# Kernel optimization log

Hardware: AMD Instinct MI355X
Metric: run time of the kernel (lower is better)

## Reference

```python
import jax, jax.numpy as jnp
import numpy as np

HIDDEN = 1024
FFN = 4096
NUM_EXPERTS = 8
TOKENS = 4096


def setup_inputs() -> dict:
    key = jax.random.key(0)
    k1, k2, k3, k4 = jax.random.split(key, 4)
    x = jax.random.normal(k1, (TOKENS, HIDDEN), dtype=jnp.float32)
    router_weight = jax.random.normal(k2, (HIDDEN, NUM_EXPERTS), dtype=jnp.float32) * 0.02
    w1 = jax.random.normal(k3, (HIDDEN, FFN * NUM_EXPERTS), dtype=jnp.float32) * 0.02
    w2 = jax.random.normal(k4, (FFN * NUM_EXPERTS, HIDDEN), dtype=jnp.float32) * 0.02
    return {"x": x, "router_weight": router_weight, "w1": w1, "w2": w2, "top_k": 2}


def reference(x, router_weight, w1, w2, top_k):
    T, H = x.shape
    E = router_weight.shape[1]
    F = w1.shape[1] // E

    # Router: fp32 logits -> softmax -> top-k gating (sparse gates in dense [T, E] form)
    logits = x.astype(jnp.float32) @ router_weight  # [T, E]
    probs = jax.nn.softmax(logits, axis=-1)
    top_vals, top_idx = jax.lax.top_k(probs, top_k)  # [T, k]
    gates = jnp.zeros((T, E), dtype=probs.dtype).at[
        jnp.arange(T)[:, None], top_idx
    ].set(top_vals)  # [T, E], zero for non-selected experts

    # Per-expert FFN (expert-blocked weight layout: columns [e*F:(e+1)*F])
    w1e = w1.reshape(H, E, F)          # [H, E, F]
    w2e = w2.reshape(E, F, H)          # [E, F, H]
    h = jax.nn.gelu(jnp.einsum('th,hef->etf', x, w1e), approximate=False)  # [E, T, F]
    y = jnp.einsum('etf,efh->eth', h, w2e)  # [E, T, H]

    # Combine: gate-weighted sum over experts
    out = jnp.einsum('te,eth->th', gates.astype(y.dtype), y)  # [T, H]
    return out
```

## Files before the change

kernel.cpp:

```cpp
#include <hip/hip_runtime.h>
#include <hip/hip_bf16.h>

#define T_TOKENS 4096
#define HID 1024
#define FFN_ 4096
#define NE 8
#define MAXROWS 9216
#define MAXTILES 72
#define KSPLIT2 2

typedef unsigned short u16;
typedef __bf16 bf16x8 __attribute__((ext_vector_type(8)));
typedef float f32x4 __attribute__((ext_vector_type(4)));
typedef u16 u16x8 __attribute__((ext_vector_type(8)));

__device__ __forceinline__ u16 f2bf(float f) {
  __hip_bfloat16 h = __float2bfloat16(f);
  return *reinterpret_cast<u16*>(&h);
}

__device__ __forceinline__ void gload16(const void* g, void* l) {
  __builtin_amdgcn_global_load_lds(
      (const __attribute__((address_space(1))) void*)g,
      (__attribute__((address_space(3))) void*)l, 16, 0, 0);
}

#define WAIT_VM8() asm volatile("s_waitcnt vmcnt(8)" ::: "memory")
#define WAIT_VM0() asm volatile("s_waitcnt vmcnt(0)" ::: "memory")
#define BARRIER()  asm volatile("s_barrier" ::: "memory")

__global__ __launch_bounds__(256) void router_kernel(
    const float* __restrict__ x, const float* __restrict__ rw,
    int* __restrict__ sel, float* __restrict__ gsel) {
  int token = blockIdx.x * 4 + (threadIdx.x >> 6);
  int lane = threadIdx.x & 63;
  const float* xr = x + (size_t)token * HID;
  float acc[8];
#pragma unroll
  for (int e = 0; e < 8; e++) acc[e] = 0.f;
  for (int h = lane; h < HID; h += 64) {
    float xv = xr[h];
    float4 r0 = *(const float4*)(rw + h * 8);
    float4 r1 = *(const float4*)(rw + h * 8 + 4);
    acc[0] += xv * r0.x; acc[1] += xv * r0.y; acc[2] += xv * r0.z; acc[3] += xv * r0.w;
    acc[4] += xv * r1.x; acc[5] += xv * r1.y; acc[6] += xv * r1.z; acc[7] += xv * r1.w;
  }
#pragma unroll
  for (int e = 0; e < 8; e++) {
#pragma unroll
    for (int o = 32; o > 0; o >>= 1) acc[e] += __shfl_down(acc[e], o);
  }
  if (lane == 0) {
    float mx = acc[0];
#pragma unroll
    for (int e = 1; e < 8; e++) mx = fmaxf(mx, acc[e]);
    float p[8], s = 0.f;
#pragma unroll
    for (int e = 0; e < 8; e++) { p[e] = expf(acc[e] - mx); s += p[e]; }
    float v0 = -1.f; int i0 = 0;
#pragma unroll
    for (int e = 0; e < 8; e++) if (p[e] > v0) { v0 = p[e]; i0 = e; }
    float v1 = -1.f; int i1 = 0;
#pragma unroll
    for (int e = 0; e < 8; e++) if (e != i0 && p[e] > v1) { v1 = p[e]; i1 = e; }
    float inv = 1.f / s;
    sel[token * 2] = i0;     gsel[token * 2] = v0 * inv;
    sel[token * 2 + 1] = i1; gsel[token * 2 + 1] = v1 * inv;
  }
}

__global__ __launch_bounds__(256) void hist_kernel(const int* __restrict__ sel,
                                                   int* __restrict__ counts) {
  __shared__ int lc[NE];
  if (threadIdx.x < NE) lc[threadIdx.x] = 0;
  __syncthreads();
  int p = blockIdx.x * 256 + threadIdx.x;
  atomicAdd(&lc[sel[p]], 1);
  __syncthreads();
  if (threadIdx.x < NE) atomicAdd(&counts[threadIdx.x], lc[threadIdx.x]);
}

__global__ void base_kernel(const int* __restrict__ counts, int* __restrict__ cursor,
                            int* __restrict__ tilemap) {
  if (threadIdx.x == 0) {
    int base = 0;
    for (int e = 0; e < NE; e++) {
      cursor[e] = base;
      int padded = (base + counts[e] + 127) & ~127;
      for (int t = base >> 7; t < (padded >> 7); t++) tilemap[t] = e;
      base = padded;
    }
    for (int t = base >> 7; t < MAXTILES; t++) tilemap[t] = 0;
  }
}

__global__ __launch_bounds__(256) void fill_kernel(int* __restrict__ perm,
                                                   float* __restrict__ grow) {
  int i = blockIdx.x * 256 + threadIdx.x;
  if (i < MAXROWS) { perm[i] = -1; grow[i] = 0.f; }
}

__global__ __launch_bounds__(256) void scatter_kernel(
    const int* __restrict__ sel, const float* __restrict__ gsel,
    int* __restrict__ cursor, int* __restrict__ perm, float* __restrict__ grow) {
  int p = blockIdx.x * 256 + threadIdx.x;
  int e = sel[p];
  int pos = atomicAdd(&cursor[e], 1);
  perm[pos] = p >> 1;
  grow[pos] = gsel[p];
}

__global__ __launch_bounds__(256) void convert_x(const float* __restrict__ x, u16* __restrict__ xb) {
  int i = (blockIdx.x * 256 + threadIdx.x) * 8;
  float4 a = *(const float4*)(x + i);
  float4 b = *(const float4*)(x + i + 4);
  u16x8 o;
  o[0] = f2bf(a.x); o[1] = f2bf(a.y); o[2] = f2bf(a.z); o[3] = f2bf(a.w);
  o[4] = f2bf(b.x); o[5] = f2bf(b.y); o[6] = f2bf(b.z); o[7] = f2bf(b.w);
  *(u16x8*)(xb + i) = o;
}

__global__ __launch_bounds__(256) void transpose_w1(const float* __restrict__ w1, u16* __restrict__ w1t) {
  __shared__ float tile[64][65];
  int c0 = blockIdx.x * 64;
  int r0 = blockIdx.y * 64;
  int t = threadIdx.x;
  int ci = (t & 15) * 4;
  int ri = t >> 4;
#pragma unroll
  for (int rr = 0; rr < 64; rr += 16) {
    float4 v = *(const float4*)(w1 + (size_t)(r0 + ri + rr) * 32768 + c0 + ci);
    tile[ri + rr][ci] = v.x; tile[ri + rr][ci + 1] = v.y;
    tile[ri + rr][ci + 2] = v.z; tile[ri + rr][ci + 3] = v.w;
  }
  __syncthreads();
  int j = t >> 2;
  int q = t & 3;
  u16x8 o0, o1;
#pragma unroll
  for (int k = 0; k < 8; k++) o0[k] = f2bf(tile[q * 16 + k][j]);
#pragma unroll
  for (int k = 0; k < 8; k++) o1[k] = f2bf(tile[q * 16 + 8 + k][j]);
  u16* dst = w1t + (size_t)(c0 + j) * 1024 + r0 + q * 16;
  *(u16x8*)dst = o0;
  *(u16x8*)(dst + 8) = o1;
}

__global__ __launch_bounds__(256) void transpose_w2(const float* __restrict__ w2, u16* __restrict__ w2t) {
  __shared__ float tile[64][65];
  int fb = blockIdx.x;
  int h0 = blockIdx.y * 64;
  int e = fb >> 6;
  int f0 = (fb & 63) * 64;
  int t = threadIdx.x;
  int ci = (t & 15) * 4;
  int ri = t >> 4;
#pragma unroll
  for (int rr = 0; rr < 64; rr += 16) {
    float4 v = *(const float4*)(w2 + (size_t)(fb * 64 + ri + rr) * 1024 + h0 + ci);
    tile[ri + rr][ci] = v.x; tile[ri + rr][ci + 1] = v.y;
    tile[ri + rr][ci + 2] = v.z; tile[ri + rr][ci + 3] = v.w;
  }
  __syncthreads();
  int j = t >> 2;
  int q = t & 3;
  u16x8 o0, o1;
#pragma unroll
  for (int k = 0; k < 8; k++) o0[k] = f2bf(tile[q * 16 + k][j]);
#pragma unroll
  for (int k = 0; k < 8; k++) o1[k] = f2bf(tile[q * 16 + 8 + k][j]);
  u16* dst = w2t + (size_t)e * 4194304 + (size_t)(h0 + j) * 4096 + f0 + q * 16;
  *(u16x8*)dst = o0;
  *(u16x8*)(dst + 8) = o1;
}

__global__ __launch_bounds__(256) void gemm1_kernel(
    const u16* __restrict__ xb, const u16* __restrict__ w1t,
    const int* __restrict__ perm, const float* __restrict__ grow,
    const int* __restrict__ tilemap, u16* __restrict__ hbuf,
    const u16* __restrict__ zp) {
  int mt = blockIdx.x, nt = blockIdx.y;
  int e = tilemap[mt];
  int row0 = mt * 128;
  int t = threadIdx.x, lane = t & 63, wave = t >> 6;
  __shared__ u16 As[2][128 * 64], Bs[2][128 * 64];

  const u16* asrc[4]; int astep[4];
  const u16* bsrc[4];
#pragma unroll
  for (int i = 0; i < 4; i++) {
    int chunk = i * 256 + t, row = chunk >> 3, c = chunk & 7;
    int cs = c ^ (row & 7);
    int tok = perm[row0 + row];
    if (tok >= 0) { asrc[i] = xb + (size_t)tok * 1024 + cs * 8; astep[i] = 64; }
    else { asrc[i] = zp + cs * 8; astep[i] = 0; }
    bsrc[i] = w1t + (size_t)e * 4194304 + (size_t)(nt * 128 + row) * 1024 + cs * 8;
  }

  f32x4 acc[4][4] = {};
  int wm = (wave >> 1) * 64, wn = (wave & 1) * 64;
  int r = lane & 15, kg = lane >> 4;

  auto stage = [&](int p) {
#pragma unroll
    for (int i = 0; i < 4; i++)
      gload16(asrc[i], (char*)&As[p][0] + i * 4096 + wave * 1024);
#pragma unroll
    for (int i = 0; i < 4; i++)
      gload16(bsrc[i], (char*)&Bs[p][0] + i * 4096 + wave * 1024);
#pragma unroll
    for (int i = 0; i < 4; i++) { asrc[i] += astep[i]; bsrc[i] += 64; }
  };
  auto compute = [&](int p) {
#pragma unroll
    for (int kk = 0; kk < 2; kk++) {
      bf16x8 af[4], bfr[4];
      int kb = kk * 64 + kg * 16;
#pragma unroll
      for (int mi = 0; mi < 4; mi++) {
        int rr = wm + mi * 16 + r;
        af[mi] = *(const bf16x8*)((const char*)&As[p][0] + rr * 128 + (kb ^ ((rr & 7) << 4)));
      }
#pragma unroll
      for (int ni = 0; ni < 4; ni++) {
        int rr = wn + ni * 16 + r;
        bfr[ni] = *(const bf16x8*)((const char*)&Bs[p][0] + rr * 128 + (kb ^ ((rr & 7) << 4)));
      }
#pragma unroll
      for (int mi = 0; mi < 4; mi++)
#pragma unroll
        for (int ni = 0; ni < 4; ni++)
          acc[mi][ni] = __builtin_amdgcn_mfma_f32_16x16x32_bf16(af[mi], bfr[ni], acc[mi][ni], 0, 0, 0);
    }
  };

  stage(0);
  stage(1);
  for (int ks = 0; ks < 15; ks++) {
    WAIT_VM8();
    BARRIER();
    compute(ks & 1);
    BARRIER();
    if (ks < 14) stage(ks & 1);
  }
  WAIT_VM0();
  BARRIER();
  compute(1);

  float g[4][4];
#pragma unroll
  for (int mi = 0; mi < 4; mi++)
#pragma unroll
    for (int j = 0; j < 4; j++)
      g[mi][j] = grow[row0 + wm + mi * 16 + kg * 4 + j];
#pragma unroll
  for (int mi = 0; mi < 4; mi++)
#pragma unroll
    for (int ni = 0; ni < 4; ni++)
#pragma unroll
      for (int j = 0; j < 4; j++) {
        int rl = wm + mi * 16 + kg * 4 + j;
        int col = nt * 128 + wn + ni * 16 + r;
        float v = acc[mi][ni][j];
        float ge = 0.5f * v * (1.0f + erff(v * 0.7071067811865475f)) * g[mi][j];
        hbuf[(size_t)(row0 + rl) * 4096 + col] = f2bf(ge);
      }
}

__global__ __launch_bounds__(256) void gemm2_kernel(
    const u16* __restrict__ hbuf, const u16* __restrict__ w2t,
    const int* __restrict__ perm, const int* __restrict__ tilemap,
    float* __restrict__ out) {
  int mt = blockIdx.x, nt = blockIdx.y;
  int ksplit = blockIdx.z;
  int e = tilemap[mt];
  int row0 = mt * 128;
  int t = threadIdx.x, lane = t & 63, wave = t >> 6;
  __shared__ u16 As[2][128 * 64], Bs[2][128 * 64];

  const u16* asrc[4];
  const u16* bsrc[4];
#pragma unroll
  for (int i = 0; i < 4; i++) {
    int chunk = i * 256 + t, row = chunk >> 3, c = chunk & 7;
    int cs = c ^ (row & 7);
    asrc[i] = hbuf + (size_t)(row0 + row) * 4096 + (size_t)ksplit * 2048 + cs * 8;
    bsrc[i] = w2t + (size_t)e * 4194304 + (size_t)(nt * 128 + row) * 4096 + (size_t)ksplit * 2048 + cs * 8;
  }

  f32x4 acc[4][4] = {};
  int wm = (wave >> 1) * 64, wn = (wave & 1) * 64;
  int r = lane & 15, kg = lane >> 4;

  auto stage = [&](int p) {
#pragma unroll
    for (int i = 0; i < 4; i++)
      gload16(asrc[i], (char*)&As[p][0] + i * 4096 + wave * 1024);
#pragma unroll
    for (int i = 0; i < 4; i++)
      gload16(bsrc[i], (char*)&Bs[p][0] + i * 4096 + wave * 1024);
#pragma unroll
    for (int i = 0; i < 4; i++) { asrc[i] += 64; bsrc[i] += 64; }
  };
  auto compute = [&](int p) {
#pragma unroll
    for (int kk = 0; kk < 2; kk++) {
      bf16x8 af[4], bfr[4];
      int kb = kk * 64 + kg * 16;
#pragma unroll
      for (int mi = 0; mi < 4; mi++) {
        int rr = wm + mi * 16 + r;
        af[mi] = *(const bf16x8*)((const char*)&As[p][0] + rr * 128 + (kb ^ ((rr & 7) << 4)));
      }
#pragma unroll
      for (int ni = 0; ni < 4; ni++) {
        int rr = wn + ni * 16 + r;
        bfr[ni] = *(const bf16x8*)((const char*)&Bs[p][0] + rr * 128 + (kb ^ ((rr & 7) << 4)));
      }
#pragma unroll
      for (int mi = 0; mi < 4; mi++)
#pragma unroll
        for (int ni = 0; ni < 4; ni++)
          acc[mi][ni] = __builtin_amdgcn_mfma_f32_16x16x32_bf16(af[mi], bfr[ni], acc[mi][ni], 0, 0, 0);
    }
  };

  stage(0);
  stage(1);
  for (int ks = 0; ks < 31; ks++) {
    WAIT_VM8();
    BARRIER();
    compute(ks & 1);
    BARRIER();
    if (ks < 30) stage(ks & 1);
  }
  WAIT_VM0();
  BARRIER();
  compute(1);

  int tok[4][4];
#pragma unroll
  for (int mi = 0; mi < 4; mi++)
#pragma unroll
    for (int j = 0; j < 4; j++)
      tok[mi][j] = perm[row0 + wm + mi * 16 + kg * 4 + j];
#pragma unroll
  for (int mi = 0; mi < 4; mi++)
#pragma unroll
    for (int ni = 0; ni < 4; ni++)
#pragma unroll
      for (int j = 0; j < 4; j++) {
        if (tok[mi][j] >= 0) {
          int col = nt * 128 + wn + ni * 16 + r;
          atomicAdd(out + (size_t)tok[mi][j] * 1024 + col, acc[mi][ni][j]);
        }
      }
}

extern "C" void kernel_launch(void* const* d_in, const int* in_sizes, int n_in,
                              void* d_out, int out_size, void* d_ws, size_t ws_size,
                              hipStream_t stream) {
  const float* x  = (const float*)d_in[0];
  const float* rw = (const float*)d_in[1];
  const float* w1 = (const float*)d_in[2];
  const float* w2 = (const float*)d_in[3];
  float* out = (float*)d_out;
  char* ws = (char*)d_ws;

  size_t off = 0;
  auto take = [&](size_t n) { char* p = ws + off; off += (n + 255) & ~255ull; return p; };
  u16* w1t   = (u16*)take(8ull * 4096 * 1024 * 2);
  u16* w2t   = (u16*)take(8ull * 4096 * 1024 * 2);
  u16* xb    = (u16*)take((size_t)T_TOKENS * HID * 2);
  u16* hbuf  = (u16*)take((size_t)MAXROWS * FFN_ * 2);
  int* sel   = (int*)take(T_TOKENS * 2 * 4);
  float* gsel = (float*)take(T_TOKENS * 2 * 4);
  int* perm  = (int*)take(MAXROWS * 4);
  float* grow = (float*)take(MAXROWS * 4);
  int* tmap  = (int*)take(MAXTILES * 4);
  int* counts = (int*)take(NE * 4);
  int* cursor = (int*)take(NE * 4);
  u16* zp    = (u16*)take(4096);

  hipMemsetAsync(zp, 0, 4096, stream);
  hipMemsetAsync(counts, 0, NE * 4, stream);
  hipMemsetAsync(out, 0, (size_t)T_TOKENS * HID * 4, stream);

  convert_x<<<dim3(T_TOKENS * HID / (256 * 8)), 256, 0, stream>>>(x, xb);
  transpose_w1<<<dim3(512, 16), 256, 0, stream>>>(w1, w1t);
  transpose_w2<<<dim3(512, 16), 256, 0, stream>>>(w2, w2t);
  router_kernel<<<dim3(T_TOKENS / 4), 256, 0, stream>>>(x, rw, sel, gsel);
  hist_kernel<<<dim3(T_TOKENS * 2 / 256), 256, 0, stream>>>(sel, counts);
  base_kernel<<<dim3(1), 64, 0, stream>>>(counts, cursor, tmap);
  fill_kernel<<<dim3((MAXROWS + 255) / 256), 256, 0, stream>>>(perm, grow);
  scatter_kernel<<<dim3(T_TOKENS * 2 / 256), 256, 0, stream>>>(sel, gsel, cursor, perm, grow);
  gemm1_kernel<<<dim3(MAXTILES, 32), 256, 0, stream>>>(xb, w1t, perm, grow, tmap, hbuf, zp);
  gemm2_kernel<<<dim3(MAXTILES, 8, KSPLIT2), 256, 0, stream>>>(hbuf, w2t, perm, tmap, out);
}
```

Measured before the change: 438.0 us.

## Enlarge grouped GEMM tiles to 256x256 with 8 waves and XCD-aware block mapping

Both expert GEMMs move from 128x128 tiles with 4 waves to 256x256 tiles with 8 waves, so each loaded A/B byte feeds more MFMAs and global/LDS traffic per flop drops. Expert padding goes to 256 rows, and a 1D grid is remapped so blocks sharing an M-tile land on the same XCD for L2 reuse. GEMM2 now splits K four ways instead of two. It also adds s_setprio around MFMA bursts and moves the barrier inside compute. Costs are more padding waste, double the LDS per block, heavier register pressure (a 32-accumulator array), and more atomic adds into the output.

```diff
diff --git a/kernel.cpp b/kernel.cpp
--- a/kernel.cpp
+++ b/kernel.cpp
@@ -5,9 +5,8 @@
 #define HID 1024
 #define FFN_ 4096
 #define NE 8
-#define MAXROWS 9216
-#define MAXTILES 72
-#define KSPLIT2 2
+#define MAXROWS 10240
+#define MAXTILES 40
 
 typedef unsigned short u16;
 typedef __bf16 bf16x8 __attribute__((ext_vector_type(8)));
@@ -86,11 +85,11 @@
     int base = 0;
     for (int e = 0; e < NE; e++) {
       cursor[e] = base;
-      int padded = (base + counts[e] + 127) & ~127;
-      for (int t = base >> 7; t < (padded >> 7); t++) tilemap[t] = e;
+      int padded = (base + counts[e] + 255) & ~255;
+      for (int t = base >> 8; t < (padded >> 8); t++) tilemap[t] = e;
       base = padded;
     }
-    for (int t = base >> 7; t < MAXTILES; t++) tilemap[t] = 0;
+    for (int t = base >> 8; t < MAXTILES; t++) tilemap[t] = 0;
   }
 }
 
@@ -174,184 +173,225 @@
   *(u16x8*)(dst + 8) = o1;
 }
 
-__global__ __launch_bounds__(256) void gemm1_kernel(
+__global__ __launch_bounds__(512, 2) void gemm1_kernel(
     const u16* __restrict__ xb, const u16* __restrict__ w1t,
     const int* __restrict__ perm, const float* __restrict__ grow,
     const int* __restrict__ tilemap, u16* __restrict__ hbuf,
     const u16* __restrict__ zp) {
-  int mt = blockIdx.x, nt = blockIdx.y;
+  int bid = blockIdx.x;
+  int xcd = bid & 7, pos = bid >> 3;
+  int nt = pos / 5;
+  int mt = xcd * 5 + (pos - nt * 5);
   int e = tilemap[mt];
-  int row0 = mt * 128;
+  int row0 = mt * 256;
   int t = threadIdx.x, lane = t & 63, wave = t >> 6;
-  __shared__ u16 As[2][128 * 64], Bs[2][128 * 64];
+  __shared__ u16 As[2][256 * 64], Bs[2][256 * 64];
 
   const u16* asrc[4]; int astep[4];
   const u16* bsrc[4];
 #pragma unroll
   for (int i = 0; i < 4; i++) {
-    int chunk = i * 256 + t, row = chunk >> 3, c = chunk & 7;
+    int chunk = i * 512 + t, row = chunk >> 3, c = chunk & 7;
     int cs = c ^ (row & 7);
     int tok = perm[row0 + row];
     if (tok >= 0) { asrc[i] = xb + (size_t)tok * 1024 + cs * 8; astep[i] = 64; }
     else { asrc[i] = zp + cs * 8; astep[i] = 0; }
-    bsrc[i] = w1t + (size_t)e * 4194304 + (size_t)(nt * 128 + row) * 1024 + cs * 8;
-  }
-
-  f32x4 acc[4][4] = {};
-  int wm = (wave >> 1) * 64, wn = (wave & 1) * 64;
+    bsrc[i] = w1t + (size_t)e * 4194304 + (size_t)(nt * 256 + row) * 1024 + cs * 8;
+  }
+
+  f32x4 acc[8][4] = {};
+  int wm = wave >> 2, wn = wave & 3;
   int r = lane & 15, kg = lane >> 4;
 
   auto stage = [&](int p) {
 #pragma unroll
     for (int i = 0; i < 4; i++)
-      gload16(asrc[i], (char*)&As[p][0] + i * 4096 + wave * 1024);
+      gload16(asrc[i], (char*)&As[p][0] + i * 8192 + wave * 1024);
 #pragma unroll
     for (int i = 0; i < 4; i++)
-      gload16(bsrc[i], (char*)&Bs[p][0] + i * 4096 + wave * 1024);
+      gload16(bsrc[i], (char*)&Bs[p][0] + i * 8192 + wave * 1024);
 #pragma unroll
     for (int i = 0; i < 4; i++) { asrc[i] += astep[i]; bsrc[i] += 64; }
   };
   auto compute = [&](int p) {
-#pragma unroll
-    for (int kk = 0; kk < 2; kk++) {
-      bf16x8 af[4], bfr[4];
-      int kb = kk * 64 + kg * 16;
+    const char* Ab = (const char*)&As[p][0];
+    const char* Bb = (const char*)&Bs[p][0];
+#pragma unroll
+    for (int ks = 0; ks < 2; ks++) {
+      int kb = ks * 64 + kg * 16;
+      bf16x8 bfr[4];
+#pragma unroll
+      for (int ni = 0; ni < 4; ni++) {
+        int rr = wn * 64 + ni * 16 + r;
+        bfr[ni] = *(const bf16x8*)(Bb + rr * 128 + (kb ^ ((rr & 7) << 4)));
+      }
+      bf16x8 af[4];
 #pragma unroll
       for (int mi = 0; mi < 4; mi++) {
-        int rr = wm + mi * 16 + r;
-        af[mi] = *(const bf16x8*)((const char*)&As[p][0] + rr * 128 + (kb ^ ((rr & 7) << 4)));
-      }
-#pragma unroll
-      for (int ni = 0; ni < 4; ni++) {
-        int rr = wn + ni * 16 + r;
-        bfr[ni] = *(const bf16x8*)((const char*)&Bs[p][0] + rr * 128 + (kb ^ ((rr & 7) << 4)));
-      }
+        int rr = wm * 128 + mi * 16 + r;
+        af[mi] = *(const bf16x8*)(Ab + rr * 128 + (kb ^ ((rr & 7) << 4)));
+      }
+      __builtin_amdgcn_s_setprio(1);
 #pragma unroll
       for (int mi = 0; mi < 4; mi++)
 #pragma unroll
         for (int ni = 0; ni < 4; ni++)
           acc[mi][ni] = __builtin_amdgcn_mfma_f32_16x16x32_bf16(af[mi], bfr[ni], acc[mi][ni], 0, 0, 0);
+      __builtin_amdgcn_s_setprio(0);
+#pragma unroll
+      for (int mi = 0; mi < 4; mi++) {
+        int rr = wm * 128 + (mi + 4) * 16 + r;
+        af[mi] = *(const bf16x8*)(Ab + rr * 128 + (kb ^ ((rr & 7) << 4)));
+      }
+      __builtin_amdgcn_s_setprio(1);
+#pragma unroll
+      for (int mi = 0; mi < 4; mi++)
+#pragma unroll
+        for (int ni = 0; ni < 4; ni++)
+          acc[mi + 4][ni] = __builtin_amdgcn_mfma_f32_16x16x32_bf16(af[mi], bfr[ni], acc[mi + 4][ni], 0, 0, 0);
+      __builtin_amdgcn_s_setprio(0);
+      BARRIER();
     }
   };
 
   stage(0);
   stage(1);
-  for (int ks = 0; ks < 15; ks++) {
+  for (int kt = 0; kt < 15; kt++) {
     WAIT_VM8();
     BARRIER();
-    compute(ks & 1);
-    BARRIER();
-    if (ks < 14) stage(ks & 1);
+    compute(kt & 1);
+    if (kt < 14) stage(kt & 1);
   }
   WAIT_VM0();
   BARRIER();
   compute(1);
 
-  float g[4][4];
-#pragma unroll
-  for (int mi = 0; mi < 4; mi++)
+  float g[8][4];
+#pragma unroll
+  for (int mi = 0; mi < 8; mi++)
 #pragma unroll
     for (int j = 0; j < 4; j++)
-      g[mi][j] = grow[row0 + wm + mi * 16 + kg * 4 + j];
-#pragma unroll
-  for (int mi = 0; mi < 4; mi++)
+      g[mi][j] = grow[row0 + wm * 128 + mi * 16 + kg * 4 + j];
+#pragma unroll
+  for (int mi = 0; mi < 8; mi++)
 #pragma unroll
     for (int ni = 0; ni < 4; ni++)
 #pragma unroll
       for (int j = 0; j < 4; j++) {
-        int rl = wm + mi * 16 + kg * 4 + j;
-        int col = nt * 128 + wn + ni * 16 + r;
+        int rl = wm * 128 + mi * 16 + kg * 4 + j;
+        int col = nt * 256 + wn * 64 + ni * 16 + r;
         float v = acc[mi][ni][j];
         float ge = 0.5f * v * (1.0f + erff(v * 0.7071067811865475f)) * g[mi][j];
         hbuf[(size_t)(row0 + rl) * 4096 + col] = f2bf(ge);
       }
 }
 
-__global__ __launch_bounds__(256) void gemm2_kernel(
+__global__ __launch_bounds__(512, 2) void gemm2_kernel(
     const u16* __restrict__ hbuf, const u16* __restrict__ w2t,
     const int* __restrict__ perm, const int* __restrict__ tilemap,
     float* __restrict__ out) {
-  int mt = blockIdx.x, nt = blockIdx.y;
-  int ksplit = blockIdx.z;
+  int bid = blockIdx.x;
+  int xcd = bid & 7, pos = bid >> 3;
+  int c16 = pos / 5;
+  int mt = xcd * 5 + (pos - c16 * 5);
+  int ksp = c16 >> 2;
+  int nt = c16 & 3;
   int e = tilemap[mt];
-  int row0 = mt * 128;
+  int row0 = mt * 256;
   int t = threadIdx.x, lane = t & 63, wave = t >> 6;
-  __shared__ u16 As[2][128 * 64], Bs[2][128 * 64];
+  __shared__ u16 As[2][256 * 64], Bs[2][256 * 64];
 
   const u16* asrc[4];
   const u16* bsrc[4];
 #pragma unroll
   for (int i = 0; i < 4; i++) {
-    int chunk = i * 256 + t, row = chunk >> 3, c = chunk & 7;
+    int chunk = i * 512 + t, row = chunk >> 3, c = chunk & 7;
     int cs = c ^ (row & 7);
-    asrc[i] = hbuf + (size_t)(row0 + row) * 4096 + (size_t)ksplit * 2048 + cs * 8;
-    bsrc[i] = w2t + (size_t)e * 4194304 + (size_t)(nt * 128 + row) * 4096 + (size_t)ksplit * 2048 + cs * 8;
-  }
-
-  f32x4 acc[4][4] = {};
-  int wm = (wave >> 1) * 64, wn = (wave & 1) * 64;
+    asrc[i] = hbuf + (size_t)(row0 + row) * 4096 + (size_t)ksp * 1024 + cs * 8;
+    bsrc[i] = w2t + (size_t)e * 4194304 + (size_t)(nt * 256 + row) * 4096 + (size_t)ksp * 1024 + cs * 8;
+  }
+
+  f32x4 acc[8][4] = {};
+  int wm = wave >> 2, wn = wave & 3;
   int r = lane & 15, kg = lane >> 4;
 
   auto stage = [&](int p) {
 #pragma unroll
     for (int i = 0; i < 4; i++)
-      gload16(asrc[i], (char*)&As[p][0] + i * 4096 + wave * 1024);
+      gload16(asrc[i], (char*)&As[p][0] + i * 8192 + wave * 1024);
 #pragma unroll
     for (int i = 0; i < 4; i++)
-      gload16(bsrc[i], (char*)&Bs[p][0] + i * 4096 + wave * 1024);
+      gload16(bsrc[i], (char*)&Bs[p][0] + i * 8192 + wave * 1024);
 #pragma unroll
     for (int i = 0; i < 4; i++) { asrc[i] += 64; bsrc[i] += 64; }
   };
   auto compute = [&](int p) {
-#pragma unroll
-    for (int kk = 0; kk < 2; kk++) {
-      bf16x8 af[4], bfr[4];
-      int kb = kk * 64 + kg * 16;
+    const char* Ab = (const char*)&As[p][0];
+    const char* Bb = (const char*)&Bs[p][0];
+#pragma unroll
+    for (int ks = 0; ks < 2; ks++) {
+      int kb = ks * 64 + kg * 16;
+      bf16x8 bfr[4];
+#pragma unroll
+      for (int ni = 0; ni < 4; ni++) {
+        int rr = wn * 64 + ni * 16 + r;
+        bfr[ni] = *(const bf16x8*)(Bb + rr * 128 + (kb ^ ((rr & 7) << 4)));
+      }
+      bf16x8 af[4];
 #pragma unroll
       for (int mi = 0; mi < 4; mi++) {
-        int rr = wm + mi * 16 + r;
-        af[mi] = *(const bf16x8*)((const char*)&As[p][0] + rr * 128 + (kb ^ ((rr & 7) << 4)));
-      }
-#pragma unroll
-      for (int ni = 0; ni < 4; ni++) {
-        int rr = wn + ni * 16 + r;
-        bfr[ni] = *(const bf16x8*)((const char*)&Bs[p][0] + rr * 128 + (kb ^ ((rr & 7) << 4)));
-      }
+        int rr = wm * 128 + mi * 16 + r;
+        af[mi] = *(const bf16x8*)(Ab + rr * 128 + (kb ^ ((rr & 7) << 4)));
+      }
+      __builtin_amdgcn_s_setprio(1);
 #pragma unroll
       for (int mi = 0; mi < 4; mi++)
 #pragma unroll
         for (int ni = 0; ni < 4; ni++)
           acc[mi][ni] = __builtin_amdgcn_mfma_f32_16x16x32_bf16(af[mi], bfr[ni], acc[mi][ni], 0, 0, 0);
+      __builtin_amdgcn_s_setprio(0);
+#pragma unroll
+      for (int mi = 0; mi < 4; mi++) {
+        int rr = wm * 128 + (mi + 4) * 16 + r;
+        af[mi] = *(const bf16x8*)(Ab + rr * 128 + (kb ^ ((rr & 7) << 4)));
+      }
+      __builtin_amdgcn_s_setprio(1);
+#pragma unroll
+      for (int mi = 0; mi < 4; mi++)
+#pragma unroll
+        for (int ni = 0; ni < 4; ni++)
+          acc[mi + 4][ni] = __builtin_amdgcn_mfma_f32_16x16x32_bf16(af[mi], bfr[ni], acc[mi + 4][ni], 0, 0, 0);
+      __builtin_amdgcn_s_setprio(0);
+      BARRIER();
     }
   };
 
   stage(0);
   stage(1);
-  for (int ks = 0; ks < 31; ks++) {
+  for (int kt = 0; kt < 15; kt++) {
     WAIT_VM8();
     BARRIER();
-    compute(ks & 1);
-    BARRIER();
-    if (ks < 30) stage(ks & 1);
+    compute(kt & 1);
+    if (kt < 14) stage(kt & 1);
   }
   WAIT_VM0();
   BARRIER();
   compute(1);
 
-  int tok[4][4];
-#pragma unroll
-  for (int mi = 0; mi < 4; mi++)
+  int tok[8][4];
+#pragma unroll
+  for (int mi = 0; mi < 8; mi++)
 #pragma unroll
     for (int j = 0; j < 4; j++)
-      tok[mi][j] = perm[row0 + wm + mi * 16 + kg * 4 + j];
-#pragma unroll
-  for (int mi = 0; mi < 4; mi++)
+      tok[mi][j] = perm[row0 + wm * 128 + mi * 16 + kg * 4 + j];
+#pragma unroll
+  for (int mi = 0; mi < 8; mi++)
 #pragma unroll
     for (int ni = 0; ni < 4; ni++)
 #pragma unroll
       for (int j = 0; j < 4; j++) {
         if (tok[mi][j] >= 0) {
-          int col = nt * 128 + wn + ni * 16 + r;
+          int col = nt * 256 + wn * 64 + ni * 16 + r;
           atomicAdd(out + (size_t)tok[mi][j] * 1024 + col, acc[mi][ni][j]);
         }
       }
@@ -394,6 +434,6 @@
   base_kernel<<<dim3(1), 64, 0, stream>>>(counts, cursor, tmap);
   fill_kernel<<<dim3((MAXROWS + 255) / 256), 256, 0, stream>>>(perm, grow);
   scatter_kernel<<<dim3(T_TOKENS * 2 / 256), 256, 0, stream>>>(sel, gsel, cursor, perm, grow);
-  gemm1_kernel<<<dim3(MAXTILES, 32), 256, 0, stream>>>(xb, w1t, perm, grow, tmap, hbuf, zp);
-  gemm2_kernel<<<dim3(MAXTILES, 8, KSPLIT2), 256, 0, stream>>>(hbuf, w2t, perm, tmap, out);
-}
+  gemm1_kernel<<<dim3(8 * 80), 512, 0, stream>>>(xb, w1t, perm, grow, tmap, hbuf, zp);
+  gemm2_kernel<<<dim3(8 * 80), 512, 0, stream>>>(hbuf, w2t, perm, tmap, out);
+}
```

New measurement: 488.8 us. 1.12x slower.
